# Performance work log

Measured on AMD Instinct MI355X. Metric: run time of the kernel, lower is better.

Reference implementation:

```python
import jax, jax.numpy as jnp
import numpy as np

N_NODES = 100000
N_EDGES = 800000
IN_C = 96
OUT_C = 64
K_HOPS = 2  # SGConv K


def setup_inputs() -> dict:
    key = jax.random.key(0)
    k1, k2, k3 = jax.random.split(key, 3)
    x = jax.random.normal(k1, (N_NODES, IN_C), dtype=jnp.float32)
    edge_index = jax.random.randint(k2, (2, N_EDGES), 0, N_NODES, dtype=jnp.int64)
    W = jax.random.normal(k3, (OUT_C, IN_C), dtype=jnp.float32) * 0.05
    b = jnp.zeros((OUT_C,), dtype=jnp.float32)
    return {"x": x, "edge_index": edge_index, "W": W, "b": b}


def reference(x, edge_index, W, b):
    N = x.shape[0]
    # GCN normalization with added self-loops (PyG SGConv default)
    loop = jnp.arange(N, dtype=edge_index.dtype)
    row = jnp.concatenate([edge_index[0], loop])  # source
    col = jnp.concatenate([edge_index[1], loop])  # destination
    deg = jax.ops.segment_sum(jnp.ones_like(col, dtype=x.dtype), col, num_segments=N)
    dinv = jnp.where(deg > 0, jax.lax.rsqrt(deg), 0.0)
    norm = dinv[row] * dinv[col]  # [E+N]
    for _ in range(K_HOPS):
        x = jax.ops.segment_sum(norm[:, None] * x[row], col, num_segments=N)
    # Linear then sigmoid
    out = x @ W.T + b
    return jax.nn.sigmoid(out)
```

## Files before the change

kernel.cpp:

```cpp
#include <hip/hip_runtime.h>
#include <hip/hip_bf16.h>
#include <math.h>

#define N_NODES 100000
#define N_EDGES 800000
#define IN_C 96
#define OUT_C 64
#define C4 (IN_C / 4)
#define XPAD 104
#define SCAN_B 512

typedef __attribute__((ext_vector_type(8))) short bf16x8;
typedef __attribute__((ext_vector_type(4))) float f32x4;

__device__ __forceinline__ unsigned short f2bf(float f) {
    unsigned u = __float_as_uint(f);
    unsigned r = 0x7FFFu + ((u >> 16) & 1u);
    return (unsigned short)((u + r) >> 16);
}
__device__ __forceinline__ unsigned pack2bf(float a, float b) {
    return (unsigned)f2bf(a) | ((unsigned)f2bf(b) << 16);
}
__device__ __forceinline__ float dec_w(unsigned p) {
    return __uint_as_float((p & 0x7FFFu) << 16);
}
__device__ __forceinline__ unsigned char f2fp8(float f) {
    return (unsigned char)(__builtin_amdgcn_cvt_pk_fp8_f32(f, f, 0, false) & 0xFF);
}

__device__ __forceinline__ void linear_block(int g, int tid,
                                             const float* __restrict__ x,
                                             const float* __restrict__ W,
                                             unsigned char* __restrict__ y, int n,
                                             unsigned short* wbf) {
    int lane = tid & 63;
    int wv = tid >> 6;
    int node0 = g * 64;

    for (int i = tid; i < 64 * C4; i += 256) {
        int o = i / C4;
        int c4 = i - o * C4;
        float4 v = ((const float4*)(W + (size_t)o * IN_C))[c4];
        uint2 pk;
        pk.x = pack2bf(v.x, v.y);
        pk.y = pack2bf(v.z, v.w);
        *(uint2*)&wbf[o * XPAD + c4 * 4] = pk;
    }
    __syncthreads();

    int l16 = lane & 15;
    int quad = lane >> 4;

    int arow = node0 + wv * 16 + l16;
    const float* xr = x + (size_t)((arow < n) ? arow : 0) * IN_C + quad * 8;

    f32x4 acc0 = {0.f, 0.f, 0.f, 0.f};
    f32x4 acc1 = {0.f, 0.f, 0.f, 0.f};
    f32x4 acc2 = {0.f, 0.f, 0.f, 0.f};
    f32x4 acc3 = {0.f, 0.f, 0.f, 0.f};

#pragma unroll
    for (int kc = 0; kc < 3; ++kc) {
        float4 v0 = ((const float4*)(xr + kc * 32))[0];
        float4 v1 = ((const float4*)(xr + kc * 32))[1];
        union { bf16x8 v; unsigned u[4]; } au;
        au.u[0] = pack2bf(v0.x, v0.y);
        au.u[1] = pack2bf(v0.z, v0.w);
        au.u[2] = pack2bf(v1.x, v1.y);
        au.u[3] = pack2bf(v1.z, v1.w);
        bf16x8 a = au.v;
        bf16x8 b0 = *(const bf16x8*)&wbf[(0 * 16 + l16) * XPAD + kc * 32 + quad * 8];
        bf16x8 b1 = *(const bf16x8*)&wbf[(1 * 16 + l16) * XPAD + kc * 32 + quad * 8];
        bf16x8 b2 = *(const bf16x8*)&wbf[(2 * 16 + l16) * XPAD + kc * 32 + quad * 8];
        bf16x8 b3 = *(const bf16x8*)&wbf[(3 * 16 + l16) * XPAD + kc * 32 + quad * 8];
        acc0 = __builtin_amdgcn_mfma_f32_16x16x32_bf16(a, b0, acc0, 0, 0, 0);
        acc1 = __builtin_amdgcn_mfma_f32_16x16x32_bf16(a, b1, acc1, 0, 0, 0);
        acc2 = __builtin_amdgcn_mfma_f32_16x16x32_bf16(a, b2, acc2, 0, 0, 0);
        acc3 = __builtin_amdgcn_mfma_f32_16x16x32_bf16(a, b3, acc3, 0, 0, 0);
    }

#pragma unroll
    for (int r = 0; r < 4; ++r) {
        int node = node0 + wv * 16 + quad * 4 + r;
        if (node < n) {
            size_t base = (size_t)node * OUT_C + l16;
            y[base + 0]  = f2fp8(acc0[r]);
            y[base + 16] = f2fp8(acc1[r]);
            y[base + 32] = f2fp8(acc2[r]);
            y[base + 48] = f2fp8(acc3[r]);
        }
    }
}

__global__ void count_linear_kernel(const int* __restrict__ col, int* __restrict__ cnt,
                                    unsigned short* __restrict__ eidx,
                                    unsigned* __restrict__ csr, int e,
                                    const float* __restrict__ x, const float* __restrict__ W,
                                    unsigned char* __restrict__ y, int n, int lin_half) {
    __shared__ unsigned short wbf[64 * XPAD];
    int g = blockIdx.x / 3;
    int r3 = blockIdx.x - g * 3;
    if (r3 != 2) {
        int i = (g * 2 + r3) * 256 + threadIdx.x;
        if (i < 16) csr[e + i] = 0u;
        if (i < e) {
            int slot = atomicAdd(&cnt[col[i]], 1);
            eidx[i] = (unsigned short)slot;
        }
        return;
    }
    if (g >= lin_half) return;
    linear_block(g, threadIdx.x, x, W, y, n, wbf);
}

__global__ void scan_pass1_kernel(const int* __restrict__ cnt, int* __restrict__ partials, int n) {
    __shared__ int s[SCAN_B];
    int i = blockIdx.x * SCAN_B + threadIdx.x;
    int v = (i < n) ? cnt[i] : 0;
    s[threadIdx.x] = v;
    __syncthreads();
    for (int off = SCAN_B / 2; off > 0; off >>= 1) {
        if (threadIdx.x < off) s[threadIdx.x] += s[threadIdx.x + off];
        __syncthreads();
    }
    if (threadIdx.x == 0) partials[blockIdx.x] = s[0];
}

__global__ void scan23_kernel(const int* __restrict__ cnt, const int* __restrict__ partials,
                              int* __restrict__ row_start, float* __restrict__ dinv,
                              int n, int nparts) {
    __shared__ int ps[SCAN_B];
    __shared__ int es[SCAN_B];
    int t = threadIdx.x;

    int pv = (t < nparts) ? partials[t] : 0;
    ps[t] = pv;
    __syncthreads();
    int run = pv;
    for (int off = 1; off < SCAN_B; off <<= 1) {
        int tmp = (t >= off) ? ps[t - off] : 0;
        __syncthreads();
        run += tmp;
        ps[t] = run;
        __syncthreads();
    }
    int total = ps[nparts - 1];
    __syncthreads();
    ps[t] = run - pv;
    __syncthreads();
    int block_off = ps[blockIdx.x];

    int i = blockIdx.x * SCAN_B + t;
    int v = (i < n) ? cnt[i] : 0;
    es[t] = v;
    __syncthreads();
    int erun = v;
    for (int off = 1; off < SCAN_B; off <<= 1) {
        int tmp = (t >= off) ? es[t - off] : 0;
        __syncthreads();
        erun += tmp;
        es[t] = erun;
        __syncthreads();
    }
    if (i < n) {
        int start = block_off + erun - v;
        row_start[i] = start;
        dinv[i] = rsqrtf((float)v + 1.0f);
    }
    if (blockIdx.x == 0 && t == 0) row_start[n] = total;
}

__global__ void fill_linear_kernel(const int* __restrict__ row, const int* __restrict__ col,
                                   const float* __restrict__ dinv,
                                   const int* __restrict__ row_start,
                                   const unsigned short* __restrict__ eidx,
                                   unsigned* __restrict__ csr, int e,
                                   const float* __restrict__ x, const float* __restrict__ W,
                                   unsigned char* __restrict__ y, int n,
                                   int lin_half, int nb_lin) {
    __shared__ unsigned short wbf[64 * XPAD];

    int g = blockIdx.x / 3;
    int r3 = blockIdx.x - g * 3;
    if (r3 != 2) {
        int i = (g * 2 + r3) * 256 + threadIdx.x;
        if (i < e) {
            int r = row[i];
            int c = col[i];
            int pos = row_start[c] + (int)eidx[i];
            csr[pos] = ((unsigned)r << 15) | (unsigned)f2bf(dinv[r]);
        }
        return;
    }
    int gl = lin_half + g;
    if (gl >= nb_lin) return;
    linear_block(gl, threadIdx.x, x, W, y, n, wbf);
}


#define GACC(EA, EB, EC, ED, w, v) \
    EA += (w) * __builtin_amdgcn_cvt_f32_fp8((int)(v), 0); \
    EB += (w) * __builtin_amdgcn_cvt_f32_fp8((int)(v), 1); \
    EC += (w) * __builtin_amdgcn_cvt_f32_fp8((int)(v), 2); \
    ED += (w) * __builtin_amdgcn_cvt_f32_fp8((int)(v), 3);

template <bool FINAL>
__global__ void gather_kernel(const unsigned char* __restrict__ src,
                              unsigned char* __restrict__ dst_fp8,
                              float* __restrict__ dst_f32,
                              const int* __restrict__ row_start, const unsigned* __restrict__ csr,
                              const float* __restrict__ dinv, const float* __restrict__ bias,
                              int n) {
    int node = blockIdx.x * (blockDim.x >> 4) + (threadIdx.x >> 4);
    if (node >= n) return;
    int c = threadIdx.x & 15;
    const unsigned* srcp = (const unsigned*)src;

    int beg = row_start[node];
    int end = row_start[node + 1];

    unsigned pv = srcp[(size_t)node * 16 + c];
    float s = dinv[node];
    float ss = s * s;

    float e0a = 0.f, e0b = 0.f, e0c = 0.f, e0d = 0.f;
    float e1a = 0.f, e1b = 0.f, e1c = 0.f, e1d = 0.f;
    float e2a = 0.f, e2b = 0.f, e2c = 0.f, e2d = 0.f;
    float e3a = 0.f, e3b = 0.f, e3c = 0.f, e3d = 0.f;
    GACC(e0a, e0b, e0c, e0d, ss, pv)

    for (int j0 = beg; j0 < end; j0 += 16) {
        unsigned t0 = csr[j0];
        unsigned t1 = csr[j0 + 1];
        unsigned t2 = csr[j0 + 2];
        unsigned t3 = csr[j0 + 3];
        unsigned t4 = csr[j0 + 4];
        unsigned t5 = csr[j0 + 5];
        unsigned t6 = csr[j0 + 6];
        unsigned t7 = csr[j0 + 7];
        unsigned t8 = csr[j0 + 8];
        unsigned t9 = csr[j0 + 9];
        unsigned ta = csr[j0 + 10];
        unsigned tb = csr[j0 + 11];
        unsigned tc = csr[j0 + 12];
        unsigned td = csr[j0 + 13];
        unsigned te = csr[j0 + 14];
        unsigned tf = csr[j0 + 15];
        unsigned p0 = (j0 + 0  < end) ? t0 : 0u;
        unsigned p1 = (j0 + 1  < end) ? t1 : 0u;
        unsigned p2 = (j0 + 2  < end) ? t2 : 0u;
        unsigned p3 = (j0 + 3  < end) ? t3 : 0u;
        unsigned p4 = (j0 + 4  < end) ? t4 : 0u;
        unsigned p5 = (j0 + 5  < end) ? t5 : 0u;
        unsigned p6 = (j0 + 6  < end) ? t6 : 0u;
        unsigned p7 = (j0 + 7  < end) ? t7 : 0u;
        unsigned p8 = (j0 + 8  < end) ? t8 : 0u;
        unsigned p9 = (j0 + 9  < end) ? t9 : 0u;
        unsigned pa = (j0 + 10 < end) ? ta : 0u;
        unsigned pb = (j0 + 11 < end) ? tb : 0u;
        unsigned pc = (j0 + 12 < end) ? tc : 0u;
        unsigned pd = (j0 + 13 < end) ? td : 0u;
        unsigned pe = (j0 + 14 < end) ? te : 0u;
        unsigned pf = (j0 + 15 < end) ? tf : 0u;
        unsigned v0 = srcp[(size_t)(p0 >> 15) * 16 + c];
        unsigned v1 = srcp[(size_t)(p1 >> 15) * 16 + c];
        unsigned v2 = srcp[(size_t)(p2 >> 15) * 16 + c];
        unsigned v3 = srcp[(size_t)(p3 >> 15) * 16 + c];
        unsigned v4 = srcp[(size_t)(p4 >> 15) * 16 + c];
        unsigned v5 = srcp[(size_t)(p5 >> 15) * 16 + c];
        unsigned v6 = srcp[(size_t)(p6 >> 15) * 16 + c];
        unsigned v7 = srcp[(size_t)(p7 >> 15) * 16 + c];
        unsigned v8 = srcp[(size_t)(p8 >> 15) * 16 + c];
        unsigned v9 = srcp[(size_t)(p9 >> 15) * 16 + c];
        unsigned va = srcp[(size_t)(pa >> 15) * 16 + c];
        unsigned vb = srcp[(size_t)(pb >> 15) * 16 + c];
        unsigned vc = srcp[(size_t)(pc >> 15) * 16 + c];
        unsigned vd = srcp[(size_t)(pd >> 15) * 16 + c];
        unsigned ve = srcp[(size_t)(pe >> 15) * 16 + c];
        unsigned vf = srcp[(size_t)(pf >> 15) * 16 + c];
        float w0 = dec_w(p0) * s, w1 = dec_w(p1) * s, w2 = dec_w(p2) * s, w3 = dec_w(p3) * s;
        float w4 = dec_w(p4) * s, w5 = dec_w(p5) * s, w6 = dec_w(p6) * s, w7 = dec_w(p7) * s;
        float w8 = dec_w(p8) * s, w9 = dec_w(p9) * s, wa = dec_w(pa) * s, wb = dec_w(pb) * s;
        float wc = dec_w(pc) * s, wd = dec_w(pd) * s, we = dec_w(pe) * s, wf = dec_w(pf) * s;
        GACC(e0a, e0b, e0c, e0d, w0, v0)
        GACC(e1a, e1b, e1c, e1d, w1, v1)
        GACC(e2a, e2b, e2c, e2d, w2, v2)
        GACC(e3a, e3b, e3c, e3d, w3, v3)
        GACC(e0a, e0b, e0c, e0d, w4, v4)
        GACC(e1a, e1b, e1c, e1d, w5, v5)
        GACC(e2a, e2b, e2c, e2d, w6, v6)
        GACC(e3a, e3b, e3c, e3d, w7, v7)
        GACC(e0a, e0b, e0c, e0d, w8, v8)
        GACC(e1a, e1b, e1c, e1d, w9, v9)
        GACC(e2a, e2b, e2c, e2d, wa, va)
        GACC(e3a, e3b, e3c, e3d, wb, vb)
        GACC(e0a, e0b, e0c, e0d, wc, vc)
        GACC(e1a, e1b, e1c, e1d, wd, vd)
        GACC(e2a, e2b, e2c, e2d, we, ve)
        GACC(e3a, e3b, e3c, e3d, wf, vf)
    }
    float a0 = (e0a + e1a) + (e2a + e3a);
    float a1 = (e0b + e1b) + (e2b + e3b);
    float a2 = (e0c + e1c) + (e2c + e3c);
    float a3 = (e0d + e1d) + (e2d + e3d);

    if (FINAL) {
        float4 bb = ((const float4*)bias)[c];
        float4 o;
        o.x = 1.0f / (1.0f + __expf(-(a0 + bb.x)));
        o.y = 1.0f / (1.0f + __expf(-(a1 + bb.y)));
        o.z = 1.0f / (1.0f + __expf(-(a2 + bb.z)));
        o.w = 1.0f / (1.0f + __expf(-(a3 + bb.w)));
        ((float4*)dst_f32)[(size_t)node * 16 + c] = o;
    } else {
        unsigned o = (unsigned)__builtin_amdgcn_cvt_pk_fp8_f32(a0, a1, 0, false);
        o = (unsigned)__builtin_amdgcn_cvt_pk_fp8_f32(a2, a3, (int)o, true);
        ((unsigned*)dst_fp8)[(size_t)node * 16 + c] = o;
    }
}


static inline size_t align16(size_t x) { return (x + 15) & ~(size_t)15; }

extern "C" void kernel_launch(void* const* d_in, const int* in_sizes, int n_in,
                              void* d_out, int out_size, void* d_ws, size_t ws_size,
                              hipStream_t stream) {
    const float* x = (const float*)d_in[0];
    const int* edge_index = (const int*)d_in[1];
    const float* W = (const float*)d_in[2];
    const float* b = (const float*)d_in[3];
    float* out = (float*)d_out;

    const int N = N_NODES;
    const int E = in_sizes[1] / 2;

    const int* row = edge_index;
    const int* col = edge_index + E;

    char* ws = (char*)d_ws;
    size_t off = 0;
    int* cnt = (int*)(ws + off);             off = align16(off + (size_t)N * 4);
    float* dinv = (float*)(ws + off);        off = align16(off + (size_t)N * 4);
    int* row_start = (int*)(ws + off);       off = align16(off + (size_t)(N + 1) * 4);
    int* partials = (int*)(ws + off);        off = align16(off + 512 * 4);
    unsigned* csr = (unsigned*)(ws + off);   off = align16(off + (size_t)(E + 16) * 4);
    unsigned char* y0 = (unsigned char*)(ws + off); off = align16(off + (size_t)N * OUT_C);
    unsigned char* y1 = (unsigned char*)(ws + off); off = align16(off + (size_t)N * OUT_C);
    unsigned short* eidx = (unsigned short*)y1;

    const int B = 256;
    const int nb_e = (E + B - 1) / B;
    const int nb_scan = (N + SCAN_B - 1) / SCAN_B;
    const int nb_lin = (N + 63) / 64;
    const int lin_half = nb_lin / 2;
    int nbg_c = (nb_e + 1) / 2;
    if (nbg_c < lin_half) nbg_c = lin_half;
    int nbg_f = (nb_e + 1) / 2;
    if (nbg_f < nb_lin - lin_half) nbg_f = nb_lin - lin_half;

    hipMemsetAsync(cnt, 0, (size_t)N * 4, stream);
    count_linear_kernel<<<3 * nbg_c, B, 0, stream>>>(col, cnt, eidx, csr, E,
                                                     x, W, y0, N, lin_half);
    scan_pass1_kernel<<<nb_scan, SCAN_B, 0, stream>>>(cnt, partials, N);
    scan23_kernel<<<nb_scan, SCAN_B, 0, stream>>>(cnt, partials, row_start, dinv, N, nb_scan);

    fill_linear_kernel<<<3 * nbg_f, B, 0, stream>>>(row, col, dinv, row_start, eidx, csr, E,
                                                    x, W, y0, N, lin_half, nb_lin);

    gather_kernel<false><<<(N + 15) / 16, B, 0, stream>>>(y0, y1, nullptr, row_start, csr, dinv, b, N);

    gather_kernel<true><<<(N + 15) / 16, B, 0, stream>>>(y1, nullptr, out, row_start, csr, dinv, b, N);
}
```

Measured before the change: 183.7 us.

## Fuse two-pass prefix scan into one kernel using atomic chunk offsets

Replaces the two scan kernels (block partial sums, then a global scan of partials plus local scan) with one kernel. Each block scans 512 counts locally and takes its base offset from an atomicAdd on a global counter. CSR segments are then no longer in node order, so the gather kernels compute the end index as row_start plus the per-node count. This removes a kernel launch and the redundant rescan of partials. The cost is an out-of-order edge layout that may reduce locality between neighbouring nodes.

```diff
diff --git a/kernel.cpp b/kernel.cpp
--- a/kernel.cpp
+++ b/kernel.cpp
@@ -8,7 +8,6 @@
 #define OUT_C 64
 #define C4 (IN_C / 4)
 #define XPAD 104
-#define SCAN_B 512
 
 typedef __attribute__((ext_vector_type(8))) short bf16x8;
 typedef __attribute__((ext_vector_type(4))) float f32x4;
@@ -113,61 +112,49 @@
     linear_block(g, threadIdx.x, x, W, y, n, wbf);
 }
 
-__global__ void scan_pass1_kernel(const int* __restrict__ cnt, int* __restrict__ partials, int n) {
-    __shared__ int s[SCAN_B];
-    int i = blockIdx.x * SCAN_B + threadIdx.x;
-    int v = (i < n) ? cnt[i] : 0;
-    s[threadIdx.x] = v;
-    __syncthreads();
-    for (int off = SCAN_B / 2; off > 0; off >>= 1) {
-        if (threadIdx.x < off) s[threadIdx.x] += s[threadIdx.x + off];
+__global__ void scan_fused_kernel(const int* __restrict__ cnt, int* __restrict__ total,
+                                  int* __restrict__ row_start, float* __restrict__ dinv,
+                                  int n) {
+    __shared__ int ss[256];
+    __shared__ int chunk_base;
+    int t = threadIdx.x;
+    int base = blockIdx.x << 9;
+
+    int i0 = base + t;
+    int v0 = (i0 < n) ? cnt[i0] : 0;
+    int r0 = v0;
+    ss[t] = v0;
+    __syncthreads();
+    for (int off = 1; off < 256; off <<= 1) {
+        int tmp = (t >= off) ? ss[t - off] : 0;
         __syncthreads();
-    }
-    if (threadIdx.x == 0) partials[blockIdx.x] = s[0];
-}
-
-__global__ void scan23_kernel(const int* __restrict__ cnt, const int* __restrict__ partials,
-                              int* __restrict__ row_start, float* __restrict__ dinv,
-                              int n, int nparts) {
-    __shared__ int ps[SCAN_B];
-    __shared__ int es[SCAN_B];
-    int t = threadIdx.x;
-
-    int pv = (t < nparts) ? partials[t] : 0;
-    ps[t] = pv;
-    __syncthreads();
-    int run = pv;
-    for (int off = 1; off < SCAN_B; off <<= 1) {
-        int tmp = (t >= off) ? ps[t - off] : 0;
+        r0 += tmp;
+        ss[t] = r0;
         __syncthreads();
-        run += tmp;
-        ps[t] = run;
+    }
+    int total0 = ss[255];
+    __syncthreads();
+
+    int i1 = base + 256 + t;
+    int v1 = (i1 < n) ? cnt[i1] : 0;
+    int r1 = v1;
+    ss[t] = v1;
+    __syncthreads();
+    for (int off = 1; off < 256; off <<= 1) {
+        int tmp = (t >= off) ? ss[t - off] : 0;
         __syncthreads();
-    }
-    int total = ps[nparts - 1];
-    __syncthreads();
-    ps[t] = run - pv;
-    __syncthreads();
-    int block_off = ps[blockIdx.x];
-
-    int i = blockIdx.x * SCAN_B + t;
-    int v = (i < n) ? cnt[i] : 0;
-    es[t] = v;
-    __syncthreads();
-    int erun = v;
-    for (int off = 1; off < SCAN_B; off <<= 1) {
-        int tmp = (t >= off) ? es[t - off] : 0;
+        r1 += tmp;
+        ss[t] = r1;
         __syncthreads();
-        erun += tmp;
-        es[t] = erun;
-        __syncthreads();
-    }
-    if (i < n) {
-        int start = block_off + erun - v;
-        row_start[i] = start;
-        dinv[i] = rsqrtf((float)v + 1.0f);
-    }
-    if (blockIdx.x == 0 && t == 0) row_start[n] = total;
+    }
+    int total1 = ss[255];
+
+    if (t == 0) chunk_base = atomicAdd(total, total0 + total1);
+    __syncthreads();
+    int b0 = chunk_base;
+
+    if (i0 < n) { row_start[i0] = b0 + r0 - v0;          dinv[i0] = rsqrtf((float)v0 + 1.0f); }
+    if (i1 < n) { row_start[i1] = b0 + total0 + r1 - v1; dinv[i1] = rsqrtf((float)v1 + 1.0f); }
 }
 
 __global__ void fill_linear_kernel(const int* __restrict__ row, const int* __restrict__ col,
@@ -208,7 +195,9 @@
 __global__ void gather_kernel(const unsigned char* __restrict__ src,
                               unsigned char* __restrict__ dst_fp8,
                               float* __restrict__ dst_f32,
-                              const int* __restrict__ row_start, const unsigned* __restrict__ csr,
+                              const int* __restrict__ row_start,
+                              const int* __restrict__ cnt,
+                              const unsigned* __restrict__ csr,
                               const float* __restrict__ dinv, const float* __restrict__ bias,
                               int n) {
     int node = blockIdx.x * (blockDim.x >> 4) + (threadIdx.x >> 4);
@@ -217,7 +206,7 @@
     const unsigned* srcp = (const unsigned*)src;
 
     int beg = row_start[node];
-    int end = row_start[node + 1];
+    int end = beg + cnt[node];
 
     unsigned pv = srcp[(size_t)node * 16 + c];
     float s = dinv[node];
@@ -340,9 +329,9 @@
     char* ws = (char*)d_ws;
     size_t off = 0;
     int* cnt = (int*)(ws + off);             off = align16(off + (size_t)N * 4);
+    int* total = (int*)(ws + off);           off = align16(off + 16);
     float* dinv = (float*)(ws + off);        off = align16(off + (size_t)N * 4);
-    int* row_start = (int*)(ws + off);       off = align16(off + (size_t)(N + 1) * 4);
-    int* partials = (int*)(ws + off);        off = align16(off + 512 * 4);
+    int* row_start = (int*)(ws + off);       off = align16(off + (size_t)N * 4);
     unsigned* csr = (unsigned*)(ws + off);   off = align16(off + (size_t)(E + 16) * 4);
     unsigned char* y0 = (unsigned char*)(ws + off); off = align16(off + (size_t)N * OUT_C);
     unsigned char* y1 = (unsigned char*)(ws + off); off = align16(off + (size_t)N * OUT_C);
@@ -350,7 +339,7 @@
 
     const int B = 256;
     const int nb_e = (E + B - 1) / B;
-    const int nb_scan = (N + SCAN_B - 1) / SCAN_B;
+    const int nb_scan = (N + 511) / 512;
     const int nb_lin = (N + 63) / 64;
     const int lin_half = nb_lin / 2;
     int nbg_c = (nb_e + 1) / 2;
@@ -358,16 +347,17 @@
     int nbg_f = (nb_e + 1) / 2;
     if (nbg_f < nb_lin - lin_half) nbg_f = nb_lin - lin_half;
 
-    hipMemsetAsync(cnt, 0, (size_t)N * 4, stream);
+    hipMemsetAsync(cnt, 0, (size_t)N * 4 + 16, stream);
+
     count_linear_kernel<<<3 * nbg_c, B, 0, stream>>>(col, cnt, eidx, csr, E,
                                                      x, W, y0, N, lin_half);
-    scan_pass1_kernel<<<nb_scan, SCAN_B, 0, stream>>>(cnt, partials, N);
-    scan23_kernel<<<nb_scan, SCAN_B, 0, stream>>>(cnt, partials, row_start, dinv, N, nb_scan);
+
+    scan_fused_kernel<<<nb_scan, B, 0, stream>>>(cnt, total, row_start, dinv, N);
 
     fill_linear_kernel<<<3 * nbg_f, B, 0, stream>>>(row, col, dinv, row_start, eidx, csr, E,
                                                     x, W, y0, N, lin_half, nb_lin);
 
-    gather_kernel<false><<<(N + 15) / 16, B, 0, stream>>>(y0, y1, nullptr, row_start, csr, dinv, b, N);
-
-    gather_kernel<true><<<(N + 15) / 16, B, 0, stream>>>(y1, nullptr, out, row_start, csr, dinv, b, N);
-}
+    gather_kernel<false><<<(N + 15) / 16, B, 0, stream>>>(y0, y1, nullptr, row_start, cnt, csr, dinv, b, N);
+
+    gather_kernel<true><<<(N + 15) / 16, B, 0, stream>>>(y1, nullptr, out, row_start, cnt, csr, dinv, b, N);
+}
```

Result: slower. 188.5 us (+2.6%).
